# Kernel optimization log

Hardware: AMD Instinct MI355X
Metric: run time of the kernel (lower is better)

Reference implementation:

```python
import jax, jax.numpy as jnp
import numpy as np

B, L, D, DF, E = 8, 2048, 256, 1024, 1


def _layer_norm(x, g, b):
    mu = jnp.mean(x, axis=-1, keepdims=True)
    var = jnp.mean((x - mu) ** 2, axis=-1, keepdims=True)
    return (x - mu) * jax.lax.rsqrt(var + 1e-5) * g + b


def _ema_scan(z, a):
    # diagonal linear SSM: h_t = a*h_{t-1} + (1-a)*z_t, scanned over seq axis
    def step(h, zt):
        h = a * h + (1.0 - a) * zt
        return h, h
    zT = jnp.swapaxes(z, 0, 1)  # [L,B,D]
    h0 = jnp.zeros((z.shape[0], z.shape[2]), z.dtype)
    _, hs = jax.lax.scan(step, h0, zT)
    return jnp.swapaxes(hs, 0, 1)


def _mamba_block(x, m, Win, a_logit, Wout):
    zg = (x * m) @ Win                      # [B,L,2D]
    z, g = jnp.split(zg, 2, axis=-1)
    h = _ema_scan(z, jax.nn.sigmoid(a_logit))
    return ((h * jax.nn.silu(g)) @ Wout) * m


def _graph_agg(x, m, A_list, We):
    out = jnp.zeros_like(x)
    for e in range(We.shape[0]):
        A = A_list[e]
        agg = jnp.einsum('bij,bjd->bid', A, x * m)  # neighbor aggregation
        deg = jnp.clip(jnp.sum(A, axis=-1, keepdims=True), 1.0, None)
        out = out + (agg / deg) @ We[e]
    return jax.nn.relu(out) * m


def _masked_gather(x, idx, vc):
    # emulate: x_out[b,:vc] = x[b, idx[b,:vc]]; x_out[b,vc:] = x[b,vc:]
    pos = jnp.arange(x.shape[1])[None, :]
    im = jnp.where(pos < vc, idx, pos)
    return jnp.take_along_axis(x, im[:, :, None], axis=1)


def _forward(node_embedding, adjacency, gm1_Win, gm1_a_logit, gm1_Wout, gm2_We,
             gm_Win, gm_a_logit, gm_Wout, gm_We, ln1_g, ln1_b, ln2_g, ln2_b,
             ffn_W1, ffn_b1, ffn_W2, ffn_b2, Wv, bv,
             node_mask, sorted_list, reverse_list):
    X = node_embedding
    m = node_mask[:, :, None].astype(X.dtype)
    vc = jnp.sum(node_mask, axis=1, keepdims=True)  # [B,1] valid counts
    A_list = [adjacency]
    outs = []
    for si, ri in zip(sorted_list, reverse_list):
        se = _masked_gather(X, si, vc)
        bo = _mamba_block(se, m, gm1_Win, gm1_a_logit, gm1_Wout)
        re = _masked_gather(bo, ri, vc)
        outs.append(_graph_agg(re, m, A_list, gm2_We))
    outs.append(_mamba_block(X, m, gm_Win, gm_a_logit, gm_Wout) +
                _graph_agg(X, m, A_list, gm_We))
    # stack(dim=-1) + permute(0,1,3,2) + reshape == concat along feature dim
    Y = jnp.concatenate(outs, axis=-1) @ Wv + bv
    X1 = X + _layer_norm(Y, ln1_g, ln1_b)        # AddNorm, pre_ln, eval (no dropout)
    Y2 = jax.nn.relu(X1 @ ffn_W1 + ffn_b1) @ ffn_W2 + ffn_b2
    return X1 + _layer_norm(Y2, ln2_g, ln2_b)


def setup_inputs() -> dict:
    key = jax.random.key(0)
    ks = jax.random.split(key, 20)
    X = jax.random.normal(ks[0], (B, L, D), jnp.float32)
    lengths = jax.random.randint(ks[1], (B,), L // 2, L + 1)
    pos = jnp.arange(L)[None, :]
    M = (pos < lengths[:, None]).astype(jnp.int32)
    A = (jax.random.uniform(ks[2], (B, L, L)) < 0.004).astype(jnp.float32)
    A = A * M[:, :, None].astype(jnp.float32) * M[:, None, :].astype(jnp.float32)
    inp = {'node_embedding': X, 'node_mask': M, 'adjacency': A}
    for i in range(3):
        u = jax.random.uniform(ks[3 + i], (B, L))
        u = jnp.where(pos < lengths[:, None], u, 2.0 + pos.astype(jnp.float32))
        si = jnp.argsort(u, axis=1).astype(jnp.int32)   # perm of [0,vc) in prefix
        ri = jnp.argsort(si, axis=1).astype(jnp.int32)  # inverse permutation
        inp['sorted_indices_%d' % i] = si
        inp['reverse_indices_%d' % i] = ri
    def w(k, shape):
        return 0.02 * jax.random.normal(k, shape, jnp.float32)
    inp.update(
        gm1_Win=w(ks[6], (D, 2 * D)), gm1_a_logit=w(ks[7], (D,)), gm1_Wout=w(ks[8], (D, D)),
        gm2_We=w(ks[9], (E, D, D)),
        gm_Win=w(ks[10], (D, 2 * D)), gm_a_logit=w(ks[11], (D,)), gm_Wout=w(ks[12], (D, D)),
        gm_We=w(ks[13], (E, D, D)),
        ln1_g=jnp.ones((D,), jnp.float32), ln1_b=jnp.zeros((D,), jnp.float32),
        ln2_g=jnp.ones((D,), jnp.float32), ln2_b=jnp.zeros((D,), jnp.float32),
        ffn_W1=w(ks[14], (D, DF)), ffn_b1=jnp.zeros((DF,), jnp.float32),
        ffn_W2=w(ks[15], (DF, D)), ffn_b2=jnp.zeros((D,), jnp.float32),
        Wv=w(ks[16], (4 * D, D)), bv=jnp.zeros((D,), jnp.float32),
    )
    return inp


def reference(node_embedding, node_mask, adjacency,
              sorted_indices_0, sorted_indices_1, sorted_indices_2,
              reverse_indices_0, reverse_indices_1, reverse_indices_2,
              gm1_Win, gm1_a_logit, gm1_Wout, gm2_We,
              gm_Win, gm_a_logit, gm_Wout, gm_We,
              ln1_g, ln1_b, ln2_g, ln2_b,
              ffn_W1, ffn_b1, ffn_W2, ffn_b2, Wv, bv):
    return _forward(node_embedding, adjacency, gm1_Win, gm1_a_logit, gm1_Wout, gm2_We,
                    gm_Win, gm_a_logit, gm_Wout, gm_We, ln1_g, ln1_b, ln2_g, ln2_b,
                    ffn_W1, ffn_b1, ffn_W2, ffn_b2, Wv, bv,
                    node_mask,
                    [sorted_indices_0, sorted_indices_1, sorted_indices_2],
                    [reverse_indices_0, reverse_indices_1, reverse_indices_2])
```

## Files before the change

kernel.cpp:

```cpp
#include <hip/hip_runtime.h>

typedef unsigned short u16;
typedef unsigned int u32;
typedef unsigned long long u64;

#define BB 8
#define LL 2048
#define DD 256
#define NB (BB * LL)
#define NBR 4
#define NRT (NBR * NB)
#define NCH 32
#define CHL (LL / NCH)
#define CAP 64

typedef __attribute__((ext_vector_type(8))) __bf16 bf16x8;
typedef __attribute__((ext_vector_type(4))) float f32x4;

__device__ __forceinline__ float b2f(u16 u) {
    union { u32 u; float f; } x; x.u = ((u32)u) << 16; return x.f;
}
__device__ __forceinline__ u16 f2b(float f) {
    union { float f; u32 u; } x; x.f = f;
    u32 r = (x.u >> 16) & 1u;
    x.u += 0x7FFFu + r;
    return (u16)(x.u >> 16);
}
__device__ __forceinline__ float sigm(float x) { return 1.f / (1.f + __expf(-x)); }

#define GLD(gp, lp) __builtin_amdgcn_global_load_lds( \
    (const __attribute__((address_space(1))) void*)(gp), \
    (__attribute__((address_space(3))) void*)(lp), 16, 0, 0)

struct TrArgs {
    const float* s[9];
    u16* d[9];
    int K[9], N[9], tr[9];
    int beg[11];
    const float* xsrc;
    const int* maskp;
    u16* xdst;
};
__global__ void transpose_all(TrArgs a) {
    int blk = blockIdx.x;
    int i = 0;
    while (blk >= a.beg[i + 1]) ++i;
    if (i == 9) {
        int g = (blk - a.beg[9]) * 256 + threadIdx.x;
        int r = g >> 6;
        float4 v = a.maskp[r] ? *(const float4*)(a.xsrc + (size_t)g * 4)
                              : (float4){0.f, 0.f, 0.f, 0.f};
        union { u64 q; u16 h[4]; } pk;
        pk.h[0] = f2b(v.x); pk.h[1] = f2b(v.y); pk.h[2] = f2b(v.z); pk.h[3] = f2b(v.w);
        *(u64*)(a.xdst + (size_t)g * 4) = pk.q;
        return;
    }
    int idx = (blk - a.beg[i]) * 256 + threadIdx.x;
    int K = a.K[i], N = a.N[i];
    if (idx >= K * N) return;
    if (a.tr[i]) {
        int k = idx / N, n = idx - k * N;
        a.d[i][(size_t)n * K + k] = f2b(a.s[i][idx]);
    } else {
        a.d[i][idx] = f2b(a.s[i][idx]);
    }
}

__global__ void csr_kernel(const float* __restrict__ Adj,
                           const int* __restrict__ ri0, const int* __restrict__ ri1,
                           const int* __restrict__ ri2,
                           int* __restrict__ csr4, int* __restrict__ cnt,
                           float* __restrict__ deg) {
    int w = threadIdx.x >> 6, lane = threadIdx.x & 63;
    int row = blockIdx.x * 4 + w;
    int rowb = row & ~(LL - 1);
    const float* arow = Adj + (size_t)row * LL;
    int base = 0;
    for (int c = 0; c < LL / 256; ++c) {
        float4 v = *(const float4*)(arow + c * 256 + lane * 4);
#pragma unroll
        for (int e = 0; e < 4; ++e) {
            float f = (e == 0) ? v.x : (e == 1) ? v.y : (e == 2) ? v.z : v.w;
            bool nz = (f != 0.f);
            u64 m = __ballot(nz);
            if (nz) {
                int pos = base + __popcll(m & ((1ull << lane) - 1ull));
                if (pos < CAP) {
                    int j = c * 256 + lane * 4 + e;
                    csr4[((size_t)(3 * NB + row)) * CAP + pos] = j;
                    csr4[((size_t)(0 * NB + row)) * CAP + pos] = ri0[rowb + j];
                    csr4[((size_t)(1 * NB + row)) * CAP + pos] = ri1[rowb + j];
                    csr4[((size_t)(2 * NB + row)) * CAP + pos] = ri2[rowb + j];
                }
            }
            base += __popcll(m);
        }
    }
    if (lane == 0) {
        cnt[row] = base < CAP ? base : CAP;
        deg[row] = (float)(base < 1 ? 1 : base);
    }
}

__global__ __launch_bounds__(256)
void gemm_win_kernel(const u16* __restrict__ Xb,
                     const int* __restrict__ si0, const int* __restrict__ si1,
                     const int* __restrict__ si2,
                     const u16* __restrict__ Bt1, const u16* __restrict__ Bt2,
                     u16* __restrict__ zbuf, u16* __restrict__ gbuf)
{
    __shared__ __align__(16) u16 As[2][128 * 32];
    __shared__ __align__(16) u16 Bs[2][128 * 32];
    int tid = threadIdx.x, lane = tid & 63;
    int w = tid >> 6, wm = w >> 1, wn = w & 1;
    int rowBase = blockIdx.x * 128, colBase = blockIdx.y * 128;
    const u16* Bt = (rowBase < 3 * NB) ? Bt1 : Bt2;

    const u16* pa[2];
    const u16* pb[2];
#pragma unroll
    for (int rep = 0; rep < 2; ++rep) {
        int s = rep * 256 + tid;
        int row = s >> 2, kk = (s & 3) << 3;
        int rg = rowBase + row;
        int br = rg >> 14, r = rg & (NB - 1), b = r >> 11, l = r & (LL - 1);
        int src = (br == 0) ? si0[r] : (br == 1) ? si1[r] : (br == 2) ? si2[r] : l;
        pa[rep] = Xb + ((size_t)(b << 11) + src) * DD + kk;
        pb[rep] = Bt + (size_t)(colBase + row) * 256 + kk;
    }

    f32x4 acc[4][4];
#pragma unroll
    for (int m = 0; m < 4; ++m)
#pragma unroll
        for (int n = 0; n < 4; ++n) acc[m][n] = (f32x4){0.f, 0.f, 0.f, 0.f};

#pragma unroll
    for (int rep = 0; rep < 2; ++rep) {
        int s = rep * 256 + tid;
        GLD(pa[rep], As[0] + s * 8);
        GLD(pb[rep], Bs[0] + s * 8);
    }
    int p = 0;
    for (int t = 0; t < 8; ++t) {
        if (t + 1 < 8) {
            int k0 = (t + 1) * 32;
#pragma unroll
            for (int rep = 0; rep < 2; ++rep) {
                int s = rep * 256 + tid;
                GLD(pa[rep] + k0, As[p ^ 1] + s * 8);
                GLD(pb[rep] + k0, Bs[p ^ 1] + s * 8);
            }
            asm volatile("s_waitcnt vmcnt(4)" ::: "memory");
        } else {
            asm volatile("s_waitcnt vmcnt(0)" ::: "memory");
        }
        __builtin_amdgcn_s_barrier();
        int kq = (lane >> 4) << 3;
        bf16x8 av[4], bw[4];
#pragma unroll
        for (int m = 0; m < 4; ++m)
            av[m] = *(const bf16x8*)(As[p] + (wm * 64 + m * 16 + (lane & 15)) * 32 + kq);
#pragma unroll
        for (int n = 0; n < 4; ++n)
            bw[n] = *(const bf16x8*)(Bs[p] + (wn * 64 + n * 16 + (lane & 15)) * 32 + kq);
#pragma unroll
        for (int m = 0; m < 4; ++m)
#pragma unroll
            for (int n = 0; n < 4; ++n)
                acc[m][n] = __builtin_amdgcn_mfma_f32_16x16x32_bf16(av[m], bw[n], acc[m][n], 0, 0, 0);
        __builtin_amdgcn_s_barrier();
        p ^= 1;
    }

    u16* Cz;
    int cb;
    if (colBase < 256) { Cz = zbuf; cb = colBase; }
    else               { Cz = gbuf; cb = colBase - 256; }
    int cBase = cb + wn * 64 + (lane & 15);
    int rBase = rowBase + wm * 64 + ((lane >> 4) << 2);
#pragma unroll
    for (int m = 0; m < 4; ++m)
#pragma unroll
        for (int n = 0; n < 4; ++n)
#pragma unroll
            for (int r = 0; r < 4; ++r)
                Cz[(size_t)(rBase + m * 16 + r) * 256 + (cBase + n * 16)] = f2b(acc[m][n][r]);
}

__global__ __launch_bounds__(256)
void gemm_kernel(const u16* __restrict__ A1, const u16* __restrict__ A2, int asplit,
                 const u16* __restrict__ Bt1, const u16* __restrict__ Bt2,
                 const u16* __restrict__ Bt3, int split1, int split2,
                 void* __restrict__ Cout, const float* __restrict__ bias,
                 int N, int K, int mode)
{
    __shared__ __align__(16) u16 As[2][128 * 32];
    __shared__ __align__(16) u16 Bs[2][128 * 32];
    int tid = threadIdx.x;
    int lane = tid & 63;
    int w = tid >> 6, wm = w >> 1, wn = w & 1;
    int rowBase = blockIdx.x * 128, colBase = blockIdx.y * 128;
    const u16* Bt = (rowBase < split1) ? Bt1 : (rowBase < split2) ? Bt2 : Bt3;
    const u16* Arow = (rowBase < asplit) ? A1 + (size_t)rowBase * K
                                         : A2 + (size_t)(rowBase - asplit) * K;

    const u16* pa[2];
    const u16* pb[2];
#pragma unroll
    for (int rep = 0; rep < 2; ++rep) {
        int s = rep * 256 + tid;
        int row = s >> 2, kk = (s & 3) << 3;
        pa[rep] = Arow + (size_t)row * K + kk;
        pb[rep] = Bt + (size_t)(colBase + row) * K + kk;
    }

    f32x4 acc[4][4];
#pragma unroll
    for (int m = 0; m < 4; ++m)
#pragma unroll
        for (int n = 0; n < 4; ++n) acc[m][n] = (f32x4){0.f, 0.f, 0.f, 0.f};

    int nt = K >> 5;
#pragma unroll
    for (int rep = 0; rep < 2; ++rep) {
        int s = rep * 256 + tid;
        GLD(pa[rep], As[0] + s * 8);
        GLD(pb[rep], Bs[0] + s * 8);
    }
    int p = 0;
    for (int t = 0; t < nt; ++t) {
        if (t + 1 < nt) {
            int k0 = (t + 1) << 5;
#pragma unroll
            for (int rep = 0; rep < 2; ++rep) {
                int s = rep * 256 + tid;
                GLD(pa[rep] + k0, As[p ^ 1] + s * 8);
                GLD(pb[rep] + k0, Bs[p ^ 1] + s * 8);
            }
            asm volatile("s_waitcnt vmcnt(4)" ::: "memory");
        } else {
            asm volatile("s_waitcnt vmcnt(0)" ::: "memory");
        }
        __builtin_amdgcn_s_barrier();
        int kq = (lane >> 4) << 3;
        bf16x8 av[4], bw[4];
#pragma unroll
        for (int m = 0; m < 4; ++m)
            av[m] = *(const bf16x8*)(As[p] + (wm * 64 + m * 16 + (lane & 15)) * 32 + kq);
#pragma unroll
        for (int n = 0; n < 4; ++n)
            bw[n] = *(const bf16x8*)(Bs[p] + (wn * 64 + n * 16 + (lane & 15)) * 32 + kq);
#pragma unroll
        for (int m = 0; m < 4; ++m)
#pragma unroll
            for (int n = 0; n < 4; ++n)
                acc[m][n] = __builtin_amdgcn_mfma_f32_16x16x32_bf16(av[m], bw[n], acc[m][n], 0, 0, 0);
        __builtin_amdgcn_s_barrier();
        p ^= 1;
    }

    int cBase = colBase + wn * 64 + (lane & 15);
    int rBase = rowBase + wm * 64 + ((lane >> 4) << 2);
    u16* C = (u16*)Cout;
    float bz[4];
#pragma unroll
    for (int n = 0; n < 4; ++n) bz[n] = bias ? bias[cBase + n * 16] : 0.f;
#pragma unroll
    for (int m = 0; m < 4; ++m)
#pragma unroll
        for (int n = 0; n < 4; ++n)
#pragma unroll
            for (int r = 0; r < 4; ++r) {
                float v = acc[m][n][r] + bz[n];
                if (mode == 1) v = v > 0.f ? v : 0.f;
                C[(size_t)(rBase + m * 16 + r) * N + (cBase + n * 16)] = f2b(v);
            }
}

__global__ __launch_bounds__(256)
void gemm_splitk2_kernel(const u16* __restrict__ A, const u16* __restrict__ Bt,
                         u16* __restrict__ C0, u16* __restrict__ C1)
{
    __shared__ __align__(16) u16 As[2][128 * 32];
    __shared__ __align__(16) u16 Bs[2][128 * 32];
    int tid = threadIdx.x;
    int lane = tid & 63;
    int w = tid >> 6, wm = w >> 1, wn = w & 1;
    int rowBase = blockIdx.x * 128, colBase = blockIdx.y * 128;
    int koff = blockIdx.z * 512;

    const u16* pa[2];
    const u16* pb[2];
#pragma unroll
    for (int rep = 0; rep < 2; ++rep) {
        int s = rep * 256 + tid;
        int row = s >> 2, kk = (s & 3) << 3;
        pa[rep] = A + (size_t)(rowBase + row) * 1024 + koff + kk;
        pb[rep] = Bt + (size_t)(colBase + row) * 1024 + koff + kk;
    }

    f32x4 acc[4][4];
#pragma unroll
    for (int m = 0; m < 4; ++m)
#pragma unroll
        for (int n = 0; n < 4; ++n) acc[m][n] = (f32x4){0.f, 0.f, 0.f, 0.f};

#pragma unroll
    for (int rep = 0; rep < 2; ++rep) {
        int s = rep * 256 + tid;
        GLD(pa[rep], As[0] + s * 8);
        GLD(pb[rep], Bs[0] + s * 8);
    }
    int p = 0;
    for (int t = 0; t < 16; ++t) {
        if (t + 1 < 16) {
            int k0 = (t + 1) << 5;
#pragma unroll
            for (int rep = 0; rep < 2; ++rep) {
                int s = rep * 256 + tid;
                GLD(pa[rep] + k0, As[p ^ 1] + s * 8);
                GLD(pb[rep] + k0, Bs[p ^ 1] + s * 8);
            }
            asm volatile("s_waitcnt vmcnt(4)" ::: "memory");
        } else {
            asm volatile("s_waitcnt vmcnt(0)" ::: "memory");
        }
        __builtin_amdgcn_s_barrier();
        int kq = (lane >> 4) << 3;
        bf16x8 av[4], bw[4];
#pragma unroll
        for (int m = 0; m < 4; ++m)
            av[m] = *(const bf16x8*)(As[p] + (wm * 64 + m * 16 + (lane & 15)) * 32 + kq);
#pragma unroll
        for (int n = 0; n < 4; ++n)
            bw[n] = *(const bf16x8*)(Bs[p] + (wn * 64 + n * 16 + (lane & 15)) * 32 + kq);
#pragma unroll
        for (int m = 0; m < 4; ++m)
#pragma unroll
            for (int n = 0; n < 4; ++n)
                acc[m][n] = __builtin_amdgcn_mfma_f32_16x16x32_bf16(av[m], bw[n], acc[m][n], 0, 0, 0);
        __builtin_amdgcn_s_barrier();
        p ^= 1;
    }

    u16* C = blockIdx.z ? C1 : C0;
    int cBase = colBase + wn * 64 + (lane & 15);
    int rBase = rowBase + wm * 64 + ((lane >> 4) << 2);
#pragma unroll
    for (int m = 0; m < 4; ++m)
#pragma unroll
        for (int n = 0; n < 4; ++n)
#pragma unroll
            for (int r = 0; r < 4; ++r)
                C[(size_t)(rBase + m * 16 + r) * 256 + (cBase + n * 16)] = f2b(acc[m][n][r]);
}

__global__ void scan_carry_kernel(const u16* __restrict__ z4, const float* __restrict__ alog1,
                                  const float* __restrict__ alog2, float* __restrict__ carry) {
    int bid = blockIdx.x;
    int br = bid >> 8, b = (bid >> 5) & 7, c = bid & 31;
    int d0 = threadIdx.x * 2;
    const float* al = (br < 3) ? alog1 : alog2;
    float aA = sigm(al[d0]), aB = sigm(al[d0 + 1]);
    float hA = 0.f, hB = 0.f;
    const u16* zp = z4 + ((size_t)(br * NB + b * LL + c * CHL) * DD) + d0;
    for (int t = 0; t < CHL; ++t) {
        u32 v = *(const u32*)(zp + (size_t)t * DD);
        hA = aA * hA + (1.f - aA) * b2f((u16)v);
        hB = aB * hB + (1.f - aB) * b2f((u16)(v >> 16));
    }
    carry[(size_t)bid * DD + d0] = hA;
    carry[(size_t)bid * DD + d0 + 1] = hB;
}

__global__ void scan_apply_kernel(const u16* __restrict__ z4, const u16* __restrict__ g4,
                                  const float* __restrict__ alog1, const float* __restrict__ alog2,
                                  const float* __restrict__ carry, u16* __restrict__ U4) {
    int bid = blockIdx.x;
    int br = bid >> 8, b = (bid >> 5) & 7, c = bid & 31;
    int d0 = threadIdx.x * 2;
    const float* al = (br < 3) ? alog1 : alog2;
    float aA = sigm(al[d0]), aB = sigm(al[d0 + 1]);
    float aPA = aA, aPB = aB;
#pragma unroll
    for (int i = 0; i < 6; ++i) { aPA *= aPA; aPB *= aPB; }
    float hA = 0.f, hB = 0.f;
    const float* cp = carry + ((size_t)((br * 8 + b) * 32)) * DD + d0;
    for (int cc = 0; cc < c; ++cc) {
        float2 cv = *(const float2*)(cp + (size_t)cc * DD);
        hA = cv.x + aPA * hA;
        hB = cv.y + aPB * hB;
    }
    size_t rowOff = ((size_t)(br * NB + b * LL + c * CHL)) * DD + d0;
    const u16* zp = z4 + rowOff;
    const u16* gp = g4 + rowOff;
    u16* up = U4 + rowOff;
    for (int t = 0; t < CHL; ++t) {
        u32 zv = *(const u32*)(zp + (size_t)t * DD);
        u32 gv = *(const u32*)(gp + (size_t)t * DD);
        float gA = b2f((u16)gv), gB = b2f((u16)(gv >> 16));
        hA = aA * hA + (1.f - aA) * b2f((u16)zv);
        hB = aB * hB + (1.f - aB) * b2f((u16)(zv >> 16));
        u32 o = (u32)f2b(hA * gA * sigm(gA)) | ((u32)f2b(hB * gB * sigm(gB)) << 16);
        *(u32*)(up + (size_t)t * DD) = o;
    }
}

__global__ void agg4_kernel(const u16* __restrict__ V5, const int* __restrict__ csr4,
                            const int* __restrict__ cnt, const float* __restrict__ deg,
                            const int* __restrict__ maskp, u16* __restrict__ Yin) {
    int tr = threadIdx.x & 31;
    int rsub = threadIdx.x >> 5;
    int rg = blockIdx.x * 8 + rsub;
    int br = rg >> 14, r = rg & (NB - 1), b = r >> 11;
    int n = cnt[r];
    const int* lst = csr4 + ((size_t)(br * NB + r)) * CAP;
    const u16* srcB = V5 + ((size_t)((br < 3 ? br : 4) * NB + (b << 11))) * DD + tr * 8;
    float acc[8] = {0.f, 0.f, 0.f, 0.f, 0.f, 0.f, 0.f, 0.f};
    int i = 0;
    for (; i + 4 <= n; i += 4) {
        int4 il = *(const int4*)(lst + i);
        union { uint4 q; u16 h[8]; } v0, v1, v2, v3;
        v0.q = *(const uint4*)(srcB + (size_t)il.x * DD);
        v1.q = *(const uint4*)(srcB + (size_t)il.y * DD);
        v2.q = *(const uint4*)(srcB + (size_t)il.z * DD);
        v3.q = *(const uint4*)(srcB + (size_t)il.w * DD);
#pragma unroll
        for (int k = 0; k < 8; ++k)
            acc[k] += b2f(v0.h[k]) + b2f(v1.h[k]) + b2f(v2.h[k]) + b2f(v3.h[k]);
    }
    for (; i < n; ++i) {
        int idx = lst[i];
        union { uint4 q; u16 h[8]; } v;
        v.q = *(const uint4*)(srcB + (size_t)idx * DD);
#pragma unroll
        for (int k = 0; k < 8; ++k) acc[k] += b2f(v.h[k]);
    }
    float inv = 1.f / deg[r];
    int msk = maskp[r];
    union { uint4 q; u16 h[8]; } mo;
    if (br == 3) mo.q = *(const uint4*)(V5 + ((size_t)(3 * NB + r)) * DD + tr * 8);
    union { uint4 q; u16 h[8]; } o;
#pragma unroll
    for (int k = 0; k < 8; ++k) {
        float v = acc[k] * inv;
        v = v > 0.f ? v : 0.f;
        if (br == 3) v += b2f(mo.h[k]);
        v = msk ? v : 0.f;
        o.h[k] = f2b(v);
    }
    *(uint4*)(Yin + (size_t)r * 1024 + (br << 8) + tr * 8) = o.q;
}

__global__ void ln1_kernel(const u16* __restrict__ Ya, const u16* __restrict__ Yb,
                           const float* __restrict__ bvp,
                           const float* __restrict__ X, const float* __restrict__ gp,
                           const float* __restrict__ bp, float* __restrict__ X1f,
                           u16* __restrict__ X1b) {
    int wv = threadIdx.x >> 6, lane = threadIdx.x & 63;
    int r = blockIdx.x * 4 + wv;
    int d0 = lane << 2;
    union { u64 q; u16 h[4]; } ya, yb;
    ya.q = *(const u64*)(Ya + (size_t)r * DD + d0);
    yb.q = *(const u64*)(Yb + (size_t)r * DD + d0);
    float4 bb = *(const float4*)(bvp + d0);
    float x[4];
#pragma unroll
    for (int k = 0; k < 4; ++k) x[k] = b2f(ya.h[k]) + b2f(yb.h[k]) + (&bb.x)[k];
    float s = x[0] + x[1] + x[2] + x[3];
#pragma unroll
    for (int o = 32; o > 0; o >>= 1) s += __shfl_xor(s, o, 64);
    float mu = s * (1.f / DD);
    float dx[4], ss = 0.f;
#pragma unroll
    for (int k = 0; k < 4; ++k) { dx[k] = x[k] - mu; ss += dx[k] * dx[k]; }
#pragma unroll
    for (int o = 32; o > 0; o >>= 1) ss += __shfl_xor(ss, o, 64);
    float rstd = rsqrtf(ss * (1.f / DD) + 1e-5f);
    float4 g4 = *(const float4*)(gp + d0);
    float4 b4 = *(const float4*)(bp + d0);
    float4 xv = *(const float4*)(X + (size_t)r * DD + d0);
    float o4[4];
    union { u64 q; u16 h[4]; } pk;
#pragma unroll
    for (int k = 0; k < 4; ++k) {
        float y = dx[k] * rstd * (&g4.x)[k] + (&b4.x)[k];
        o4[k] = (&xv.x)[k] + y;
        pk.h[k] = f2b(o4[k]);
    }
    *(float4*)(X1f + (size_t)r * DD + d0) = (float4){o4[0], o4[1], o4[2], o4[3]};
    *(u64*)(X1b + (size_t)r * DD + d0) = pk.q;
}

__global__ void ln2_kernel(const u16* __restrict__ Ya, const u16* __restrict__ Yb,
                           const float* __restrict__ b2p,
                           const float* __restrict__ X1f, const float* __restrict__ gp,
                           const float* __restrict__ bp, float* __restrict__ Out) {
    int wv = threadIdx.x >> 6, lane = threadIdx.x & 63;
    int r = blockIdx.x * 4 + wv;
    int d0 = lane << 2;
    union { u64 q; u16 h[4]; } ya, yb;
    ya.q = *(const u64*)(Ya + (size_t)r * DD + d0);
    yb.q = *(const u64*)(Yb + (size_t)r * DD + d0);
    float4 bb = *(const float4*)(b2p + d0);
    float x[4];
#pragma unroll
    for (int k = 0; k < 4; ++k) x[k] = b2f(ya.h[k]) + b2f(yb.h[k]) + (&bb.x)[k];
    float s = x[0] + x[1] + x[2] + x[3];
#pragma unroll
    for (int o = 32; o > 0; o >>= 1) s += __shfl_xor(s, o, 64);
    float mu = s * (1.f / DD);
    float dx[4], ss = 0.f;
#pragma unroll
    for (int k = 0; k < 4; ++k) { dx[k] = x[k] - mu; ss += dx[k] * dx[k]; }
#pragma unroll
    for (int o = 32; o > 0; o >>= 1) ss += __shfl_xor(ss, o, 64);
    float rstd = rsqrtf(ss * (1.f / DD) + 1e-5f);
    float4 g4 = *(const float4*)(gp + d0);
    float4 b4 = *(const float4*)(bp + d0);
    float4 xv = *(const float4*)(X1f + (size_t)r * DD + d0);
    float o4[4];
#pragma unroll
    for (int k = 0; k < 4; ++k)
        o4[k] = (&xv.x)[k] + dx[k] * rstd * (&g4.x)[k] + (&b4.x)[k];
    *(float4*)(Out + (size_t)r * DD + d0) = (float4){o4[0], o4[1], o4[2], o4[3]};
}

extern "C" void kernel_launch(void* const* d_in, const int* in_sizes, int n_in,
                              void* d_out, int out_size, void* d_ws, size_t ws_size,
                              hipStream_t stream) {
    const float* X      = (const float*)d_in[0];
    const int* maskp    = (const int*)d_in[1];
    const float* Adj    = (const float*)d_in[2];
    const int* si[3]    = { (const int*)d_in[3], (const int*)d_in[5], (const int*)d_in[7] };
    const int* ri[3]    = { (const int*)d_in[4], (const int*)d_in[6], (const int*)d_in[8] };
    const float* gm1_Win  = (const float*)d_in[9];
    const float* gm1_alog = (const float*)d_in[10];
    const float* gm1_Wout = (const float*)d_in[11];
    const float* gm2_We   = (const float*)d_in[12];
    const float* gm_Win   = (const float*)d_in[13];
    const float* gm_alog  = (const float*)d_in[14];
    const float* gm_Wout  = (const float*)d_in[15];
    const float* gm_We    = (const float*)d_in[16];
    const float* ln1_g    = (const float*)d_in[17];
    const float* ln1_b    = (const float*)d_in[18];
    const float* ln2_g    = (const float*)d_in[19];
    const float* ln2_b    = (const float*)d_in[20];
    const float* ffn_W1   = (const float*)d_in[21];
    const float* ffn_b1   = (const float*)d_in[22];
    const float* ffn_W2   = (const float*)d_in[23];
    const float* ffn_b2   = (const float*)d_in[24];
    const float* Wv       = (const float*)d_in[25];
    const float* bv       = (const float*)d_in[26];
    float* Out = (float*)d_out;

    char* ws = (char*)d_ws;
    size_t off = 0;
    auto alloc = [&](size_t bytes) { size_t o = off; off += (bytes + 255) & ~(size_t)255; return o; };

    u16* WinT1  = (u16*)(ws + alloc((size_t)512 * 256 * 2));
    u16* WinT   = (u16*)(ws + alloc((size_t)512 * 256 * 2));
    u16* WoutT  = (u16*)(ws + alloc((size_t)256 * 256 * 2));
    u16* WeT1   = (u16*)(ws + alloc((size_t)256 * 256 * 2));
    u16* WeT    = (u16*)(ws + alloc((size_t)256 * 256 * 2));
    u16* WvT    = (u16*)(ws + alloc((size_t)256 * 1024 * 2));
    u16* W1T    = (u16*)(ws + alloc((size_t)1024 * 256 * 2));
    u16* W2T    = (u16*)(ws + alloc((size_t)256 * 1024 * 2));
    u16* WoutL  = (u16*)(ws + alloc((size_t)256 * 256 * 2));
    u16* Wc1T   = (u16*)(ws + alloc((size_t)256 * 256 * 2));
    u16* Xb     = (u16*)(ws + alloc((size_t)NB * DD * 2));
    int* csr4 = (int*)(ws + alloc((size_t)4 * NB * CAP * 4));
    int* cnt = (int*)(ws + alloc((size_t)NB * 4));
    float* deg = (float*)(ws + alloc((size_t)NB * 4));
    float* carry = (float*)(ws + alloc((size_t)NBR * BB * NCH * DD * 4));
    u16* zbuf = (u16*)(ws + alloc((size_t)NRT * DD * 2));
    u16* gbuf = (u16*)(ws + alloc((size_t)NRT * DD * 2));
    u16* U4   = (u16*)(ws + alloc((size_t)4 * NB * DD * 2));
    u16* V5   = (u16*)(ws + alloc((size_t)5 * NB * DD * 2));
    u16* Yin  = (u16*)(ws + alloc((size_t)NB * 1024 * 2));
    u16* tmpYa  = (u16*)(ws + alloc((size_t)NB * DD * 2));
    u16* tmpYb  = (u16*)(ws + alloc((size_t)NB * DD * 2));
    float* X1f   = (float*)(ws + alloc((size_t)NB * DD * 4));
    u16* X1b     = (u16*)(ws + alloc((size_t)NB * DD * 2));
    u16* H       = (u16*)(ws + alloc((size_t)NB * 1024 * 2));
    u16* tmpY2a  = (u16*)(ws + alloc((size_t)NB * DD * 2));
    u16* tmpY2b  = (u16*)(ws + alloc((size_t)NB * DD * 2));
    (void)ws_size; (void)in_sizes; (void)n_in; (void)out_size;

    TrArgs ta;
    const float* srcs[9] = { gm1_Win, gm_Win, gm_Wout, gm2_We, gm_We, Wv, ffn_W1, ffn_W2, gm1_Wout };
    u16* dsts[9]         = { WinT1,   WinT,   WoutT,   WeT1,   WeT,   WvT, W1T,   W2T,    WoutL };
    int Ks[9] = { 256, 256, 256, 256, 256, 1024, 256, 1024, 256 };
    int Ns[9] = { 512, 512, 256, 256, 256, 256, 1024, 256, 256 };
    int trs[9] = { 1, 1, 1, 1, 1, 1, 1, 1, 0 };
    int cum = 0;
    for (int i = 0; i < 9; ++i) {
        ta.s[i] = srcs[i]; ta.d[i] = dsts[i]; ta.K[i] = Ks[i]; ta.N[i] = Ns[i]; ta.tr[i] = trs[i];
        ta.beg[i] = cum; cum += (Ks[i] * Ns[i]) / 256;
    }
    ta.beg[9] = cum; cum += NB * DD / 4 / 256;
    ta.beg[10] = cum;
    ta.xsrc = X; ta.maskp = maskp; ta.xdst = Xb;
    transpose_all<<<cum, 256, 0, stream>>>(ta);

    gemm_kernel<<<dim3(2, 2), 256, 0, stream>>>(
        WeT1, WeT1, 1 << 30, WoutL, WoutL, WoutL, 1 << 30, 1 << 30,
        (void*)Wc1T, nullptr, 256, 256, 2);

    csr_kernel<<<NB / 4, 256, 0, stream>>>(Adj, ri[0], ri[1], ri[2], csr4, cnt, deg);

    gemm_win_kernel<<<dim3(NRT / 128, 512 / 128), 256, 0, stream>>>(
        Xb, si[0], si[1], si[2], WinT1, WinT, zbuf, gbuf);

    scan_carry_kernel<<<NBR * BB * NCH, 128, 0, stream>>>(zbuf, gm1_alog, gm_alog, carry);
    scan_apply_kernel<<<NBR * BB * NCH, 128, 0, stream>>>(zbuf, gbuf, gm1_alog, gm_alog, carry, U4);

    gemm_kernel<<<dim3(5 * NB / 128, 2), 256, 0, stream>>>(
        U4, Xb, 4 * NB, Wc1T, WoutT, WeT, 3 * NB, 4 * NB,
        (void*)V5, nullptr, 256, 256, 2);

    agg4_kernel<<<NRT / 8, 256, 0, stream>>>(V5, csr4, cnt, deg, maskp, Yin);

    gemm_splitk2_kernel<<<dim3(NB / 128, 2, 2), 256, 0, stream>>>(Yin, WvT, tmpYa, tmpYb);

    ln1_kernel<<<NB / 4, 256, 0, stream>>>(tmpYa, tmpYb, bv, X, ln1_g, ln1_b, X1f, X1b);

    gemm_kernel<<<dim3(NB / 128, 8), 256, 0, stream>>>(
        X1b, X1b, 1 << 30, W1T, W1T, W1T, 1 << 30, 1 << 30,
        (void*)H, ffn_b1, 1024, 256, 1);

    gemm_splitk2_kernel<<<dim3(NB / 128, 2, 2), 256, 0, stream>>>(H, W2T, tmpY2a, tmpY2b);

    ln2_kernel<<<NB / 4, 256, 0, stream>>>(tmpY2a, tmpY2b, ffn_b2, X1f, ln2_g, ln2_b, Out);
}
```

Measured before the change: 257.5 us.

## Merge CSR build into prolog, widen scan kernels, drop fp32 residual buffer

```diff
diff --git a/kernel.cpp b/kernel.cpp
--- a/kernel.cpp
+++ b/kernel.cpp
@@ -32,19 +32,54 @@
     (const __attribute__((address_space(1))) void*)(gp), \
     (__attribute__((address_space(3))) void*)(lp), 16, 0, 0)
 
-struct TrArgs {
+struct PrologArgs {
     const float* s[9];
     u16* d[9];
     int K[9], N[9], tr[9];
-    int beg[11];
+    int beg[12];
     const float* xsrc;
     const int* maskp;
     u16* xdst;
+    const float* Adj;
+    const int* ri0; const int* ri1; const int* ri2;
+    int* csr4; int* cnt; float* deg;
 };
-__global__ void transpose_all(TrArgs a) {
+__global__ void prolog_kernel(PrologArgs a) {
     int blk = blockIdx.x;
     int i = 0;
     while (blk >= a.beg[i + 1]) ++i;
+    if (i == 10) {
+        int w = threadIdx.x >> 6, lane = threadIdx.x & 63;
+        int row = (blk - a.beg[10]) * 4 + w;
+        int rowb = row & ~(LL - 1);
+        const float* arow = a.Adj + (size_t)row * LL;
+        int base = 0;
+        for (int c = 0; c < LL / 256; ++c) {
+            float4 v = *(const float4*)(arow + c * 256 + lane * 4);
+#pragma unroll
+            for (int e = 0; e < 4; ++e) {
+                float f = (e == 0) ? v.x : (e == 1) ? v.y : (e == 2) ? v.z : v.w;
+                bool nz = (f != 0.f);
+                u64 m = __ballot(nz);
+                if (nz) {
+                    int pos = base + __popcll(m & ((1ull << lane) - 1ull));
+                    if (pos < CAP) {
+                        int j = c * 256 + lane * 4 + e;
+                        a.csr4[((size_t)(3 * NB + row)) * CAP + pos] = j;
+                        a.csr4[((size_t)(0 * NB + row)) * CAP + pos] = a.ri0[rowb + j];
+                        a.csr4[((size_t)(1 * NB + row)) * CAP + pos] = a.ri1[rowb + j];
+                        a.csr4[((size_t)(2 * NB + row)) * CAP + pos] = a.ri2[rowb + j];
+                    }
+                }
+                base += __popcll(m);
+            }
+        }
+        if (lane == 0) {
+            a.cnt[row] = base < CAP ? base : CAP;
+            a.deg[row] = (float)(base < 1 ? 1 : base);
+        }
+        return;
+    }
     if (i == 9) {
         int g = (blk - a.beg[9]) * 256 + threadIdx.x;
         int r = g >> 6;
@@ -63,42 +98,6 @@
         a.d[i][(size_t)n * K + k] = f2b(a.s[i][idx]);
     } else {
         a.d[i][idx] = f2b(a.s[i][idx]);
-    }
-}
-
-__global__ void csr_kernel(const float* __restrict__ Adj,
-                           const int* __restrict__ ri0, const int* __restrict__ ri1,
-                           const int* __restrict__ ri2,
-                           int* __restrict__ csr4, int* __restrict__ cnt,
-                           float* __restrict__ deg) {
-    int w = threadIdx.x >> 6, lane = threadIdx.x & 63;
-    int row = blockIdx.x * 4 + w;
-    int rowb = row & ~(LL - 1);
-    const float* arow = Adj + (size_t)row * LL;
-    int base = 0;
-    for (int c = 0; c < LL / 256; ++c) {
-        float4 v = *(const float4*)(arow + c * 256 + lane * 4);
-#pragma unroll
-        for (int e = 0; e < 4; ++e) {
-            float f = (e == 0) ? v.x : (e == 1) ? v.y : (e == 2) ? v.z : v.w;
-            bool nz = (f != 0.f);
-            u64 m = __ballot(nz);
-            if (nz) {
-                int pos = base + __popcll(m & ((1ull << lane) - 1ull));
-                if (pos < CAP) {
-                    int j = c * 256 + lane * 4 + e;
-                    csr4[((size_t)(3 * NB + row)) * CAP + pos] = j;
-                    csr4[((size_t)(0 * NB + row)) * CAP + pos] = ri0[rowb + j];
-                    csr4[((size_t)(1 * NB + row)) * CAP + pos] = ri1[rowb + j];
-                    csr4[((size_t)(2 * NB + row)) * CAP + pos] = ri2[rowb + j];
-                }
-            }
-            base += __popcll(m);
-        }
-    }
-    if (lane == 0) {
-        cnt[row] = base < CAP ? base : CAP;
-        deg[row] = (float)(base < 1 ? 1 : base);
     }
 }
 
@@ -358,52 +357,64 @@
 
 __global__ void scan_carry_kernel(const u16* __restrict__ z4, const float* __restrict__ alog1,
                                   const float* __restrict__ alog2, float* __restrict__ carry) {
-    int bid = blockIdx.x;
-    int br = bid >> 8, b = (bid >> 5) & 7, c = bid & 31;
-    int d0 = threadIdx.x * 2;
+    int chunk = blockIdx.x * 4 + (threadIdx.x >> 6);
+    int br = chunk >> 8, b = (chunk >> 5) & 7, c = chunk & 31;
+    int lane = threadIdx.x & 63;
+    int d0 = lane << 2;
     const float* al = (br < 3) ? alog1 : alog2;
-    float aA = sigm(al[d0]), aB = sigm(al[d0 + 1]);
-    float hA = 0.f, hB = 0.f;
+    float a0 = sigm(al[d0]), a1 = sigm(al[d0 + 1]), a2 = sigm(al[d0 + 2]), a3 = sigm(al[d0 + 3]);
+    float h0 = 0.f, h1 = 0.f, h2 = 0.f, h3 = 0.f;
     const u16* zp = z4 + ((size_t)(br * NB + b * LL + c * CHL) * DD) + d0;
     for (int t = 0; t < CHL; ++t) {
-        u32 v = *(const u32*)(zp + (size_t)t * DD);
-        hA = aA * hA + (1.f - aA) * b2f((u16)v);
-        hB = aB * hB + (1.f - aB) * b2f((u16)(v >> 16));
-    }
-    carry[(size_t)bid * DD + d0] = hA;
-    carry[(size_t)bid * DD + d0 + 1] = hB;
+        union { u64 q; u16 h[4]; } v;
+        v.q = *(const u64*)(zp + (size_t)t * DD);
+        h0 = a0 * h0 + (1.f - a0) * b2f(v.h[0]);
+        h1 = a1 * h1 + (1.f - a1) * b2f(v.h[1]);
+        h2 = a2 * h2 + (1.f - a2) * b2f(v.h[2]);
+        h3 = a3 * h3 + (1.f - a3) * b2f(v.h[3]);
+    }
+    *(float4*)(carry + (size_t)chunk * DD + d0) = (float4){h0, h1, h2, h3};
 }
 
 __global__ void scan_apply_kernel(const u16* __restrict__ z4, const u16* __restrict__ g4,
                                   const float* __restrict__ alog1, const float* __restrict__ alog2,
                                   const float* __restrict__ carry, u16* __restrict__ U4) {
-    int bid = blockIdx.x;
-    int br = bid >> 8, b = (bid >> 5) & 7, c = bid & 31;
-    int d0 = threadIdx.x * 2;
+    int chunk = blockIdx.x * 4 + (threadIdx.x >> 6);
+    int br = chunk >> 8, b = (chunk >> 5) & 7, c = chunk & 31;
+    int lane = threadIdx.x & 63;
+    int d0 = lane << 2;
     const float* al = (br < 3) ? alog1 : alog2;
-    float aA = sigm(al[d0]), aB = sigm(al[d0 + 1]);
-    float aPA = aA, aPB = aB;
-#pragma unroll
-    for (int i = 0; i < 6; ++i) { aPA *= aPA; aPB *= aPB; }
-    float hA = 0.f, hB = 0.f;
+    float a0 = sigm(al[d0]), a1 = sigm(al[d0 + 1]), a2 = sigm(al[d0 + 2]), a3 = sigm(al[d0 + 3]);
+    float aP0 = a0, aP1 = a1, aP2 = a2, aP3 = a3;
+#pragma unroll
+    for (int i = 0; i < 6; ++i) { aP0 *= aP0; aP1 *= aP1; aP2 *= aP2; aP3 *= aP3; }
+    float h0 = 0.f, h1 = 0.f, h2 = 0.f, h3 = 0.f;
     const float* cp = carry + ((size_t)((br * 8 + b) * 32)) * DD + d0;
     for (int cc = 0; cc < c; ++cc) {
-        float2 cv = *(const float2*)(cp + (size_t)cc * DD);
-        hA = cv.x + aPA * hA;
-        hB = cv.y + aPB * hB;
+        float4 cv = *(const float4*)(cp + (size_t)cc * DD);
+        h0 = cv.x + aP0 * h0;
+        h1 = cv.y + aP1 * h1;
+        h2 = cv.z + aP2 * h2;
+        h3 = cv.w + aP3 * h3;
     }
     size_t rowOff = ((size_t)(br * NB + b * LL + c * CHL)) * DD + d0;
     const u16* zp = z4 + rowOff;
     const u16* gp = g4 + rowOff;
     u16* up = U4 + rowOff;
     for (int t = 0; t < CHL; ++t) {
-        u32 zv = *(const u32*)(zp + (size_t)t * DD);
-        u32 gv = *(const u32*)(gp + (size_t)t * DD);
-        float gA = b2f((u16)gv), gB = b2f((u16)(gv >> 16));
-        hA = aA * hA + (1.f - aA) * b2f((u16)zv);
-        hB = aB * hB + (1.f - aB) * b2f((u16)(zv >> 16));
-        u32 o = (u32)f2b(hA * gA * sigm(gA)) | ((u32)f2b(hB * gB * sigm(gB)) << 16);
-        *(u32*)(up + (size_t)t * DD) = o;
+        union { u64 q; u16 h[4]; } zv, gv, o;
+        zv.q = *(const u64*)(zp + (size_t)t * DD);
+        gv.q = *(const u64*)(gp + (size_t)t * DD);
+        float g0 = b2f(gv.h[0]), g1 = b2f(gv.h[1]), g2 = b2f(gv.h[2]), g3 = b2f(gv.h[3]);
+        h0 = a0 * h0 + (1.f - a0) * b2f(zv.h[0]);
+        h1 = a1 * h1 + (1.f - a1) * b2f(zv.h[1]);
+        h2 = a2 * h2 + (1.f - a2) * b2f(zv.h[2]);
+        h3 = a3 * h3 + (1.f - a3) * b2f(zv.h[3]);
+        o.h[0] = f2b(h0 * g0 * sigm(g0));
+        o.h[1] = f2b(h1 * g1 * sigm(g1));
+        o.h[2] = f2b(h2 * g2 * sigm(g2));
+        o.h[3] = f2b(h3 * g3 * sigm(g3));
+        *(u64*)(up + (size_t)t * DD) = o.q;
     }
 }
 
@@ -456,8 +467,7 @@
 __global__ void ln1_kernel(const u16* __restrict__ Ya, const u16* __restrict__ Yb,
                            const float* __restrict__ bvp,
                            const float* __restrict__ X, const float* __restrict__ gp,
-                           const float* __restrict__ bp, float* __restrict__ X1f,
-                           u16* __restrict__ X1b) {
+                           const float* __restrict__ bp, u16* __restrict__ X1b) {
     int wv = threadIdx.x >> 6, lane = threadIdx.x & 63;
     int r = blockIdx.x * 4 + wv;
     int d0 = lane << 2;
@@ -481,28 +491,26 @@
     float4 g4 = *(const float4*)(gp + d0);
     float4 b4 = *(const float4*)(bp + d0);
     float4 xv = *(const float4*)(X + (size_t)r * DD + d0);
-    float o4[4];
     union { u64 q; u16 h[4]; } pk;
 #pragma unroll
     for (int k = 0; k < 4; ++k) {
         float y = dx[k] * rstd * (&g4.x)[k] + (&b4.x)[k];
-        o4[k] = (&xv.x)[k] + y;
-        pk.h[k] = f2b(o4[k]);
-    }
-    *(float4*)(X1f + (size_t)r * DD + d0) = (float4){o4[0], o4[1], o4[2], o4[3]};
+        pk.h[k] = f2b((&xv.x)[k] + y);
+    }
     *(u64*)(X1b + (size_t)r * DD + d0) = pk.q;
 }
 
 __global__ void ln2_kernel(const u16* __restrict__ Ya, const u16* __restrict__ Yb,
                            const float* __restrict__ b2p,
-                           const float* __restrict__ X1f, const float* __restrict__ gp,
+                           const u16* __restrict__ X1b, const float* __restrict__ gp,
                            const float* __restrict__ bp, float* __restrict__ Out) {
     int wv = threadIdx.x >> 6, lane = threadIdx.x & 63;
     int r = blockIdx.x * 4 + wv;
     int d0 = lane << 2;
-    union { u64 q; u16 h[4]; } ya, yb;
+    union { u64 q; u16 h[4]; } ya, yb, x1;
     ya.q = *(const u64*)(Ya + (size_t)r * DD + d0);
     yb.q = *(const u64*)(Yb + (size_t)r * DD + d0);
+    x1.q = *(const u64*)(X1b + (size_t)r * DD + d0);
     float4 bb = *(const float4*)(b2p + d0);
     float x[4];
 #pragma unroll
@@ -519,11 +527,10 @@
     float rstd = rsqrtf(ss * (1.f / DD) + 1e-5f);
     float4 g4 = *(const float4*)(gp + d0);
     float4 b4 = *(const float4*)(bp + d0);
-    float4 xv = *(const float4*)(X1f + (size_t)r * DD + d0);
     float o4[4];
 #pragma unroll
     for (int k = 0; k < 4; ++k)
-        o4[k] = (&xv.x)[k] + dx[k] * rstd * (&g4.x)[k] + (&b4.x)[k];
+        o4[k] = b2f(x1.h[k]) + dx[k] * rstd * (&g4.x)[k] + (&b4.x)[k];
     *(float4*)(Out + (size_t)r * DD + d0) = (float4){o4[0], o4[1], o4[2], o4[3]};
 }
 
@@ -581,14 +588,13 @@
     u16* Yin  = (u16*)(ws + alloc((size_t)NB * 1024 * 2));
     u16* tmpYa  = (u16*)(ws + alloc((size_t)NB * DD * 2));
     u16* tmpYb  = (u16*)(ws + alloc((size_t)NB * DD * 2));
-    float* X1f   = (float*)(ws + alloc((size_t)NB * DD * 4));
-    u16* X1b     = (u16*)(ws + alloc((size_t)NB * DD * 2));
-    u16* H       = (u16*)(ws + alloc((size_t)NB * 1024 * 2));
-    u16* tmpY2a  = (u16*)(ws + alloc((size_t)NB * DD * 2));
-    u16* tmpY2b  = (u16*)(ws + alloc((size_t)NB * DD * 2));
+    u16* X1b    = (u16*)(ws + alloc((size_t)NB * DD * 2));
+    u16* H      = (u16*)(ws + alloc((size_t)NB * 1024 * 2));
+    u16* tmpY2a = (u16*)(ws + alloc((size_t)NB * DD * 2));
+    u16* tmpY2b = (u16*)(ws + alloc((size_t)NB * DD * 2));
     (void)ws_size; (void)in_sizes; (void)n_in; (void)out_size;
 
-    TrArgs ta;
+    PrologArgs ta;
     const float* srcs[9] = { gm1_Win, gm_Win, gm_Wout, gm2_We, gm_We, Wv, ffn_W1, ffn_W2, gm1_Wout };
     u16* dsts[9]         = { WinT1,   WinT,   WoutT,   WeT1,   WeT,   WvT, W1T,   W2T,    WoutL };
     int Ks[9] = { 256, 256, 256, 256, 256, 1024, 256, 1024, 256 };
@@ -600,21 +606,22 @@
         ta.beg[i] = cum; cum += (Ks[i] * Ns[i]) / 256;
     }
     ta.beg[9] = cum; cum += NB * DD / 4 / 256;
-    ta.beg[10] = cum;
+    ta.beg[10] = cum; cum += NB / 4;
+    ta.beg[11] = cum;
     ta.xsrc = X; ta.maskp = maskp; ta.xdst = Xb;
-    transpose_all<<<cum, 256, 0, stream>>>(ta);
+    ta.Adj = Adj; ta.ri0 = ri[0]; ta.ri1 = ri[1]; ta.ri2 = ri[2];
+    ta.csr4 = csr4; ta.cnt = cnt; ta.deg = deg;
+    prolog_kernel<<<cum, 256, 0, stream>>>(ta);
 
     gemm_kernel<<<dim3(2, 2), 256, 0, stream>>>(
         WeT1, WeT1, 1 << 30, WoutL, WoutL, WoutL, 1 << 30, 1 << 30,
         (void*)Wc1T, nullptr, 256, 256, 2);
 
-    csr_kernel<<<NB / 4, 256, 0, stream>>>(Adj, ri[0], ri[1], ri[2], csr4, cnt, deg);
-
     gemm_win_kernel<<<dim3(NRT / 128, 512 / 128), 256, 0, stream>>>(
         Xb, si[0], si[1], si[2], WinT1, WinT, zbuf, gbuf);
 
-    scan_carry_kernel<<<NBR * BB * NCH, 128, 0, stream>>>(zbuf, gm1_alog, gm_alog, carry);
-    scan_apply_kernel<<<NBR * BB * NCH, 128, 0, stream>>>(zbuf, gbuf, gm1_alog, gm_alog, carry, U4);
+    scan_carry_kernel<<<NBR * BB * NCH / 4, 256, 0, stream>>>(zbuf, gm1_alog, gm_alog, carry);
+    scan_apply_kernel<<<NBR * BB * NCH / 4, 256, 0, stream>>>(zbuf, gbuf, gm1_alog, gm_alog, carry, U4);
 
     gemm_kernel<<<dim3(5 * NB / 128, 2), 256, 0, stream>>>(
         U4, Xb, 4 * NB, Wc1T, WoutT, WeT, 3 * NB, 4 * NB,
@@ -624,7 +631,7 @@
 
     gemm_splitk2_kernel<<<dim3(NB / 128, 2, 2), 256, 0, stream>>>(Yin, WvT, tmpYa, tmpYb);
 
-    ln1_kernel<<<NB / 4, 256, 0, stream>>>(tmpYa, tmpYb, bv, X, ln1_g, ln1_b, X1f, X1b);
+    ln1_kernel<<<NB / 4, 256, 0, stream>>>(tmpYa, tmpYb, bv, X, ln1_g, ln1_b, X1b);
 
     gemm_kernel<<<dim3(NB / 128, 8), 256, 0, stream>>>(
         X1b, X1b, 1 << 30, W1T, W1T, W1T, 1 << 30, 1 << 30,
@@ -632,5 +639,5 @@
 
     gemm_splitk2_kernel<<<dim3(NB / 128, 2, 2), 256, 0, stream>>>(H, W2T, tmpY2a, tmpY2b);
 
-    ln2_kernel<<<NB / 4, 256, 0, stream>>>(tmpY2a, tmpY2b, ffn_b2, X1f, ln2_g, ln2_b, Out);
-}
+    ln2_kernel<<<NB / 4, 256, 0, stream>>>(tmpY2a, tmpY2b, ffn_b2, X1b, ln2_g, ln2_b, Out);
+}
```

Result: slower. 265.0 us (+2.9%).
